# Kernel tuning notes

Hardware: AMD Instinct MI355X
Metric: run time of the kernel (lower is better)

The kernel has to match this reference:

```python
import jax, jax.numpy as jnp
import numpy as np

OHNM_RATIO = 30
DEFAULT_NEG_PERC = 0.1
EPS = 1e-10


def setup_inputs() -> dict:
    key = jax.random.key(0)
    k1, k2 = jax.random.split(key)
    shape = (1, 1, 256, 256, 256)  # (B, C, D, H, W) 3D segmentation volume
    preds = jax.random.normal(k1, shape, dtype=jnp.float32)  # raw logits
    targs = (jax.random.uniform(k2, shape, dtype=jnp.float32) < 1e-3).astype(jnp.int32)
    return {"preds": preds, "targs": targs}


def reference(preds, targs):
    t = targs.astype(preds.dtype)
    # elementwise BCE-with-logits: log(1 + e^x) - x * t  (numerically stable via logaddexp)
    losses = jnp.logaddexp(0.0, preds) - preds * t
    pf, tf, lf = preds.ravel(), t.ravel(), losses.ravel()

    # --- data-dependent hard-negative count (mirrors torch .item() host sync) ---
    n_pos = int(np.asarray(tf.sum()))
    n_neg = tf.size - n_pos
    n_hns = int(DEFAULT_NEG_PERC * n_neg) if n_pos == 0 else min(n_pos * OHNM_RATIO, n_neg)

    # mask out positives, take top-k hardest negatives over the flattened loss map
    masked = jnp.where(tf == 1.0, 0.0, lf)
    _, hns_idxs = jax.lax.top_k(masked, n_hns)
    # positive indices (data-dependent size, like torch.nonzero)
    pos_idxs = jnp.asarray(np.nonzero(np.asarray(tf) == 1.0)[0], dtype=hns_idxs.dtype)
    idxs = jnp.concatenate([hns_idxs, pos_idxs])  # [n_hns + n_pos]

    # gather selected samples, view as (B, C, -1) with B = C = 1
    ps = jax.nn.sigmoid(pf[idxs])[None, None, :]  # dice normalizes preds
    ts = tf[idxs][None, None, :]

    # Dice loss over dims 2+ (here the single flattened sample dim)
    inter = jnp.sum(ps * ts, axis=-1)              # [B, C]
    denom = jnp.sum(ps, axis=-1) + jnp.sum(ts, axis=-1)
    dice = jnp.mean(1.0 - (2.0 * inter + EPS) / (denom + EPS))

    return dice + jnp.mean(lf[idxs])
```

## Files before the change

kernel.cpp:

```cpp
#include <hip/hip_runtime.h>

#define EPSF 1e-10f

constexpr unsigned KEY15 = 0xBFC00000u;
constexpr int BUCK0 = 0xBFC;
constexpr int NB2   = 4096 - BUCK0;
constexpr int NBKT  = 4096;
constexpr int NREP  = 8;
constexpr int LHSZ  = NB2 + 64;

typedef float pf4 __attribute__((ext_vector_type(4)));
typedef int   pi4 __attribute__((ext_vector_type(4)));

constexpr int SC_OFF    = 0;
constexpr int BSTAT_OFF = 64;
constexpr int REP_OFF   = BSTAT_OFF + 4096 * 4;
constexpr int LOW_OFF   = REP_OFF + NREP * NB2;
constexpr int HF_OFF    = LOW_OFF + NBKT;
constexpr int ZERO_WORDS = LOW_OFF + NBKT;

__device__ __forceinline__ float sigmoidf_(float x) {
    return 1.0f / (1.0f + expf(-x));
}
__device__ __forceinline__ float softplusf_(float x) {
    return fmaxf(x, 0.0f) + log1pf(expf(-fabsf(x)));
}
__device__ __forceinline__ unsigned f2key(float x) {
    unsigned b = __float_as_uint(x);
    return b ^ ((unsigned)((int)b >> 31) | 0x80000000u);
}
__device__ __forceinline__ float key2f(unsigned k) {
    unsigned b = (k & 0x80000000u) ? (k & 0x7FFFFFFFu) : ~k;
    return __uint_as_float(b);
}

__global__ void zeroAll(unsigned* ws, int nwords) {
    int stride = gridDim.x * blockDim.x;
    for (int i = blockIdx.x * blockDim.x + threadIdx.x; i < nwords; i += stride)
        ws[i] = 0u;
}

__global__ __launch_bounds__(256) void k1(const float* __restrict__ preds,
                                          const int* __restrict__ targs, int N,
                                          float4* __restrict__ bstat,
                                          unsigned* __restrict__ rep) {
    __shared__ int lh[LHSZ];
    for (int i = threadIdx.x; i < LHSZ; i += 256) lh[i] = 0;
    __syncthreads();

    float pc = 0.f, psig = 0.f, plos = 0.f;
    const int tid = threadIdx.x;
    const int lane = tid & 63;
    const int w = tid >> 6;
    const int dummy = NB2 + lane;

    int nfull = N >> 13;
    for (int grp = blockIdx.x; grp < nfull; grp += gridDim.x) {
        size_t ebase = ((size_t)grp << 13) + ((size_t)w << 11) + ((size_t)lane << 2);
        const float* pp  = preds + ebase;
        const float* pp2 = pp + 1024;
        const int*   tp  = targs + ebase;
        const int*   tp2 = tp + 1024;
        pf4 P[8]; pi4 T[8];
        asm volatile(
            "global_load_dwordx4 %0, %16, off\n\t"
            "global_load_dwordx4 %1, %16, off offset:1024\n\t"
            "global_load_dwordx4 %2, %16, off offset:2048\n\t"
            "global_load_dwordx4 %3, %16, off offset:3072\n\t"
            "global_load_dwordx4 %4, %17, off\n\t"
            "global_load_dwordx4 %5, %17, off offset:1024\n\t"
            "global_load_dwordx4 %6, %17, off offset:2048\n\t"
            "global_load_dwordx4 %7, %17, off offset:3072\n\t"
            "global_load_dwordx4 %8, %18, off\n\t"
            "global_load_dwordx4 %9, %18, off offset:1024\n\t"
            "global_load_dwordx4 %10, %18, off offset:2048\n\t"
            "global_load_dwordx4 %11, %18, off offset:3072\n\t"
            "global_load_dwordx4 %12, %19, off\n\t"
            "global_load_dwordx4 %13, %19, off offset:1024\n\t"
            "global_load_dwordx4 %14, %19, off offset:2048\n\t"
            "global_load_dwordx4 %15, %19, off offset:3072\n\t"
            "s_waitcnt vmcnt(0)"
            : "=&v"(P[0]), "=&v"(P[1]), "=&v"(P[2]), "=&v"(P[3]),
              "=&v"(P[4]), "=&v"(P[5]), "=&v"(P[6]), "=&v"(P[7]),
              "=&v"(T[0]), "=&v"(T[1]), "=&v"(T[2]), "=&v"(T[3]),
              "=&v"(T[4]), "=&v"(T[5]), "=&v"(T[6]), "=&v"(T[7])
            : "v"(pp), "v"(pp2), "v"(tp), "v"(tp2)
            : "memory");
#pragma unroll
        for (int g = 0; g < 8; g++) {
            pf4 pv = P[g]; pi4 tv = T[g];
#pragma unroll
            for (int j = 0; j < 4; j++) {
                float x = pv[j];
                unsigned key = f2key(x);
                int bkt = (int)(key >> 20) - BUCK0;
                bool q = (key >= KEY15) & (tv[j] == 0);
                int addr = q ? bkt : dummy;
                atomicAdd(&lh[addr], 1);
            }
            if (tv[0] | tv[1] | tv[2] | tv[3]) {
#pragma unroll
                for (int j = 0; j < 4; j++)
                    if (tv[j]) {
                        float x = pv[j];
                        pc += 1.f; psig += sigmoidf_(x); plos += softplusf_(x) - x;
                    }
            }
        }
    }
    if (blockIdx.x == gridDim.x - 1) {
        for (int i = (nfull << 13) + tid; i < N; i += 256) {
            float x = preds[i];
            if (targs[i]) { pc += 1.f; psig += sigmoidf_(x); plos += softplusf_(x) - x; }
            else {
                unsigned key = f2key(x);
                if (key >= KEY15) atomicAdd(&lh[(key >> 20) - BUCK0], 1);
            }
        }
    }
    __syncthreads();
    float qc = 0.f;
    unsigned* my = rep + (unsigned)(blockIdx.x & (NREP - 1)) * NB2;
    for (int i = tid; i < NB2; i += 256) {
        int c = lh[i];
        if (c) { atomicAdd(&my[i], (unsigned)c); qc += (float)c; }
    }
#pragma unroll
    for (int o = 32; o > 0; o >>= 1) {
        pc   += __shfl_down(pc, o);
        psig += __shfl_down(psig, o);
        plos += __shfl_down(plos, o);
        qc   += __shfl_down(qc, o);
    }
    __shared__ float rp[4], rs[4], rl[4], rq[4];
    if ((tid & 63) == 0) { rp[w] = pc; rs[w] = psig; rl[w] = plos; rq[w] = qc; }
    __syncthreads();
    if (tid == 0)
        bstat[blockIdx.x] = make_float4(rp[0] + rp[1] + rp[2] + rp[3],
                                        rs[0] + rs[1] + rs[2] + rs[3],
                                        rl[0] + rl[1] + rl[2] + rl[3],
                                        rq[0] + rq[1] + rq[2] + rq[3]);
}

__global__ void flagK(const float4* __restrict__ bstat, int nblocks,
                      unsigned* __restrict__ sc, unsigned N) {
    float pc = 0.f, ps = 0.f, pl = 0.f, qt = 0.f;
    for (int i = threadIdx.x; i < nblocks; i += 256) {
        float4 v = bstat[i];
        pc += v.x; ps += v.y; pl += v.z; qt += v.w;
    }
#pragma unroll
    for (int o = 32; o > 0; o >>= 1) {
        pc += __shfl_down(pc, o);
        ps += __shfl_down(ps, o);
        pl += __shfl_down(pl, o);
        qt += __shfl_down(qt, o);
    }
    __shared__ float rp[4], rs[4], rl[4], rq[4];
    int w = threadIdx.x >> 6;
    if ((threadIdx.x & 63) == 0) { rp[w] = pc; rs[w] = ps; rl[w] = pl; rq[w] = qt; }
    __syncthreads();
    if (threadIdx.x == 0) {
        unsigned np = (unsigned)(rp[0] + rp[1] + rp[2] + rp[3] + 0.5f);
        float psT = rs[0] + rs[1] + rs[2] + rs[3];
        float plT = rl[0] + rl[1] + rl[2] + rl[3];
        unsigned qtT = (unsigned)(rq[0] + rq[1] + rq[2] + rq[3] + 0.5f);
        unsigned nn = N - np;
        unsigned k = (np == 0u) ? (unsigned)(0.1 * (double)nn)
                                : ((30u * np < nn) ? 30u * np : nn);
        float* scf = (float*)sc;
        sc[0] = np; scf[1] = psT; scf[2] = plT; sc[3] = k;
        sc[7] = (k > qtT) ? 1u : 0u;
    }
}

__global__ void redR(const unsigned* __restrict__ rep, unsigned* __restrict__ histF) {
    int i = blockIdx.x * 256 + threadIdx.x;
    if (i < NB2) {
        unsigned s0 = rep[0 * NB2 + i], s1 = rep[1 * NB2 + i];
        unsigned s2 = rep[2 * NB2 + i], s3 = rep[3 * NB2 + i];
        unsigned s4 = rep[4 * NB2 + i], s5 = rep[5 * NB2 + i];
        unsigned s6 = rep[6 * NB2 + i], s7 = rep[7 * NB2 + i];
        histF[i] = ((s0 + s1) + (s2 + s3)) + ((s4 + s5) + (s6 + s7));
    }
}

__global__ __launch_bounds__(256) void lowH(const float* __restrict__ preds,
                                            const int* __restrict__ targs, int N,
                                            const unsigned* __restrict__ sc,
                                            unsigned* __restrict__ low) {
    if (sc[7] == 0u) return;
    int gtid = blockIdx.x * 256 + threadIdx.x;
    int gstr = gridDim.x * 256;
    for (int i = gtid; i < N; i += gstr) {
        if (!targs[i]) {
            unsigned key = f2key(preds[i]);
            if (key < KEY15) atomicAdd(&low[key >> 20], 1u);
        }
    }
}

__global__ void finalize(const unsigned* __restrict__ histF,
                         const unsigned* __restrict__ low,
                         unsigned* __restrict__ sc, float* __restrict__ out) {
    __shared__ unsigned sa[256], sb[256];
    __shared__ int sb1;
    __shared__ unsigned sr1;
    __shared__ double rds[4], rdl[4];
    int t = threadIdx.x;
    int base = t * 16;
    unsigned c[16]; unsigned tot = 0;
#pragma unroll
    for (int j = 0; j < 16; j++) {
        int b = base + j;
        unsigned s = (b >= BUCK0) ? histF[b - BUCK0] : low[b];
        c[j] = s; tot += s;
    }
    sa[t] = tot;
    if (t == 0) { sb1 = NBKT; sr1 = 0u; }
    __syncthreads();
    unsigned k = sc[3];
    unsigned* src = sa; unsigned* dst = sb;
    for (int off = 1; off < 256; off <<= 1) {
        unsigned v = src[t] + ((t + off < 256) ? src[t + off] : 0u);
        dst[t] = v;
        __syncthreads();
        unsigned* tmp = src; src = dst; dst = tmp;
    }
    if (k > 0u) {
        unsigned above = src[t] - tot;
        if (above < k && above + tot >= k) {
            unsigned cum = above;
            for (int j = 15; j >= 0; j--) {
                unsigned cc = c[j];
                if (cum + cc >= k) { sb1 = base + j; sr1 = k - cum; break; }
                cum += cc;
            }
        }
    }
    __syncthreads();
    int b1 = sb1; unsigned r1 = sr1;
    double ssig = 0.0, ssp = 0.0;
#pragma unroll
    for (int j = 0; j < 16; j++) {
        int b = base + j; unsigned cc = c[j];
        if (cc == 0u) continue;
        bool full = (b > b1);
        bool part = (b == b1) && (r1 > 0u);
        if (!(full || part)) continue;
        float lo = key2f((unsigned)b << 20);
        float hi = (b == NBKT - 1) ? key2f(0xFF7FFFFFu)
                                   : key2f(((unsigned)(b + 1)) << 20);
        if (full) {
            float mid = 0.5f * (lo + hi);
            ssig += (double)cc * (double)sigmoidf_(mid);
            ssp  += (double)cc * (double)softplusf_(mid);
        } else {
            unsigned take = (r1 < cc) ? r1 : cc;
            double q = (double)take / (double)cc;
            float rp = (float)((double)hi - 0.5 * q * ((double)hi - (double)lo));
            ssig += (double)take * (double)sigmoidf_(rp);
            ssp  += (double)take * (double)softplusf_(rp);
        }
    }
#pragma unroll
    for (int o = 32; o > 0; o >>= 1) {
        ssig += __shfl_down(ssig, o);
        ssp  += __shfl_down(ssp, o);
    }
    int w = t >> 6;
    if ((t & 63) == 0) { rds[w] = ssig; rdl[w] = ssp; }
    __syncthreads();
    if (t == 0) {
        double sns = rds[0] + rds[1] + rds[2] + rds[3];
        double snl = rdl[0] + rdl[1] + rdl[2] + rdl[3];
        float* scf = (float*)sc;
        unsigned np = sc[0];
        float psig = scf[1], plos = scf[2];
        double denom = (double)psig + sns + (double)np;
        double dice = 1.0 - (2.0 * (double)psig + (double)EPSF) / (denom + (double)EPSF);
        unsigned totsel = np + k;
        double mean = totsel ? (((double)plos + snl) / (double)totsel) : 0.0;
        out[0] = (float)(dice + mean);
    }
}

extern "C" void kernel_launch(void* const* d_in, const int* in_sizes, int n_in,
                              void* d_out, int out_size, void* d_ws, size_t ws_size,
                              hipStream_t stream) {
    const float* preds = (const float*)d_in[0];
    const int*   targs = (const int*)d_in[1];
    float* out = (float*)d_out;
    int N = in_sizes[0];

    unsigned* ws    = (unsigned*)d_ws;
    unsigned* sc    = ws + SC_OFF;
    float4*   bstat = (float4*)(ws + BSTAT_OFF);
    unsigned* rep   = ws + REP_OFF;
    unsigned* low   = ws + LOW_OFF;
    unsigned* histF = ws + HF_OFF;

    int nfull = N >> 13;
    int grid = nfull + ((N & 8191) ? 1 : 0);
    if (grid < 1) grid = 1;
    if (grid > 4096) grid = 4096;

    zeroAll<<<64, 256, 0, stream>>>(ws, ZERO_WORDS);
    k1<<<grid, 256, 0, stream>>>(preds, targs, N, bstat, rep);
    flagK<<<1, 256, 0, stream>>>(bstat, grid, sc, (unsigned)N);
    lowH<<<512, 256, 0, stream>>>(preds, targs, N, sc, low);
    redR<<<(NB2 + 255) / 256, 256, 0, stream>>>(rep, histF);
    finalize<<<1, 256, 0, stream>>>(histF, low, sc, out);
}
```

Baseline: 161.3 us.

## Fuse histogram, flag, reduction and finalize into one last-block kernel

Merges the main histogram pass, the count/flag kernel, the replica reduction, the low-bucket fallback and the finalize step into a single kernel. The last block to finish, detected with an atomic ticket counter, performs all the tail work. This removes four kernel launches and the gaps between them. In exchange, the rare fallback scan over the low buckets now runs over all N elements in one block instead of 512 blocks. The block also carries a larger shared-memory footprint, which may reduce occupancy of the main pass.

```diff
diff --git a/kernel.cpp b/kernel.cpp
--- a/kernel.cpp
+++ b/kernel.cpp
@@ -16,8 +16,8 @@
 constexpr int BSTAT_OFF = 64;
 constexpr int REP_OFF   = BSTAT_OFF + 4096 * 4;
 constexpr int LOW_OFF   = REP_OFF + NREP * NB2;
-constexpr int HF_OFF    = LOW_OFF + NBKT;
-constexpr int ZERO_WORDS = LOW_OFF + NBKT;
+constexpr int ZERO_N    = NREP * NB2 + NBKT;
+constexpr int ZERO_TOT  = 64 + ZERO_N;
 
 __device__ __forceinline__ float sigmoidf_(float x) {
     return 1.0f / (1.0f + expf(-x));
@@ -34,17 +34,32 @@
     return __uint_as_float(b);
 }
 
-__global__ void zeroAll(unsigned* ws, int nwords) {
-    int stride = gridDim.x * blockDim.x;
-    for (int i = blockIdx.x * blockDim.x + threadIdx.x; i < nwords; i += stride)
-        ws[i] = 0u;
-}
-
-__global__ __launch_bounds__(256) void k1(const float* __restrict__ preds,
-                                          const int* __restrict__ targs, int N,
-                                          float4* __restrict__ bstat,
-                                          unsigned* __restrict__ rep) {
+__global__ void zeroAll(unsigned* ws) {
+    int stride = gridDim.x * 256;
+    for (int i = blockIdx.x * 256 + threadIdx.x; i < ZERO_TOT; i += stride)
+        ws[(i < 64) ? i : (REP_OFF - 64 + i)] = 0u;
+}
+
+__global__ __launch_bounds__(256) void fused(const float* __restrict__ preds,
+                                             const int* __restrict__ targs, int N,
+                                             unsigned* __restrict__ ws,
+                                             float* __restrict__ out) {
     __shared__ int lh[LHSZ];
+    __shared__ float rp[4], rs[4], rl[4], rq[4];
+    __shared__ unsigned histH[NB2];
+    __shared__ unsigned sa[256], sb[256];
+    __shared__ int sb1;
+    __shared__ unsigned sr1;
+    __shared__ double rds[4], rdl[4];
+    __shared__ int s_last;
+    __shared__ unsigned s_np, s_k, s_flag;
+    __shared__ float s_psig, s_plos;
+
+    unsigned* sc    = ws + SC_OFF;
+    float4*   bstat = (float4*)(ws + BSTAT_OFF);
+    unsigned* rep   = ws + REP_OFF;
+    unsigned* low   = ws + LOW_OFF;
+
     for (int i = threadIdx.x; i < LHSZ; i += 256) lh[i] = 0;
     __syncthreads();
 
@@ -132,156 +147,144 @@
         plos += __shfl_down(plos, o);
         qc   += __shfl_down(qc, o);
     }
-    __shared__ float rp[4], rs[4], rl[4], rq[4];
     if ((tid & 63) == 0) { rp[w] = pc; rs[w] = psig; rl[w] = plos; rq[w] = qc; }
     __syncthreads();
-    if (tid == 0)
+    if (tid == 0) {
         bstat[blockIdx.x] = make_float4(rp[0] + rp[1] + rp[2] + rp[3],
                                         rs[0] + rs[1] + rs[2] + rs[3],
                                         rl[0] + rl[1] + rl[2] + rl[3],
                                         rq[0] + rq[1] + rq[2] + rq[3]);
-}
-
-__global__ void flagK(const float4* __restrict__ bstat, int nblocks,
-                      unsigned* __restrict__ sc, unsigned N) {
-    float pc = 0.f, ps = 0.f, pl = 0.f, qt = 0.f;
-    for (int i = threadIdx.x; i < nblocks; i += 256) {
-        float4 v = bstat[i];
-        pc += v.x; ps += v.y; pl += v.z; qt += v.w;
-    }
-#pragma unroll
-    for (int o = 32; o > 0; o >>= 1) {
-        pc += __shfl_down(pc, o);
-        ps += __shfl_down(ps, o);
-        pl += __shfl_down(pl, o);
-        qt += __shfl_down(qt, o);
-    }
-    __shared__ float rp[4], rs[4], rl[4], rq[4];
-    int w = threadIdx.x >> 6;
-    if ((threadIdx.x & 63) == 0) { rp[w] = pc; rs[w] = ps; rl[w] = pl; rq[w] = qt; }
-    __syncthreads();
-    if (threadIdx.x == 0) {
-        unsigned np = (unsigned)(rp[0] + rp[1] + rp[2] + rp[3] + 0.5f);
-        float psT = rs[0] + rs[1] + rs[2] + rs[3];
-        float plT = rl[0] + rl[1] + rl[2] + rl[3];
-        unsigned qtT = (unsigned)(rq[0] + rq[1] + rq[2] + rq[3] + 0.5f);
-        unsigned nn = N - np;
-        unsigned k = (np == 0u) ? (unsigned)(0.1 * (double)nn)
-                                : ((30u * np < nn) ? 30u * np : nn);
-        float* scf = (float*)sc;
-        sc[0] = np; scf[1] = psT; scf[2] = plT; sc[3] = k;
-        sc[7] = (k > qtT) ? 1u : 0u;
-    }
-}
-
-__global__ void redR(const unsigned* __restrict__ rep, unsigned* __restrict__ histF) {
-    int i = blockIdx.x * 256 + threadIdx.x;
-    if (i < NB2) {
+        __threadfence();
+        unsigned t = atomicAdd(&sc[0], 1u);
+        s_last = (t == gridDim.x - 1) ? 1 : 0;
+    }
+    __syncthreads();
+    if (!s_last) return;
+    __threadfence();
+
+    {
+        float fpc = 0.f, fps = 0.f, fpl = 0.f, fqt = 0.f;
+        for (int i = tid; i < (int)gridDim.x; i += 256) {
+            float4 v = bstat[i];
+            fpc += v.x; fps += v.y; fpl += v.z; fqt += v.w;
+        }
+#pragma unroll
+        for (int o = 32; o > 0; o >>= 1) {
+            fpc += __shfl_down(fpc, o);
+            fps += __shfl_down(fps, o);
+            fpl += __shfl_down(fpl, o);
+            fqt += __shfl_down(fqt, o);
+        }
+        if ((tid & 63) == 0) { rp[w] = fpc; rs[w] = fps; rl[w] = fpl; rq[w] = fqt; }
+        __syncthreads();
+        if (tid == 0) {
+            unsigned np = (unsigned)(rp[0] + rp[1] + rp[2] + rp[3] + 0.5f);
+            float psT = rs[0] + rs[1] + rs[2] + rs[3];
+            float plT = rl[0] + rl[1] + rl[2] + rl[3];
+            unsigned qtT = (unsigned)(rq[0] + rq[1] + rq[2] + rq[3] + 0.5f);
+            unsigned nn = (unsigned)N - np;
+            unsigned k = (np == 0u) ? (unsigned)(0.1 * (double)nn)
+                                    : ((30u * np < nn) ? 30u * np : nn);
+            s_np = np; s_psig = psT; s_plos = plT; s_k = k;
+            s_flag = (k > qtT) ? 1u : 0u;
+        }
+        __syncthreads();
+    }
+
+    for (int i = tid; i < NB2; i += 256) {
         unsigned s0 = rep[0 * NB2 + i], s1 = rep[1 * NB2 + i];
         unsigned s2 = rep[2 * NB2 + i], s3 = rep[3 * NB2 + i];
         unsigned s4 = rep[4 * NB2 + i], s5 = rep[5 * NB2 + i];
         unsigned s6 = rep[6 * NB2 + i], s7 = rep[7 * NB2 + i];
-        histF[i] = ((s0 + s1) + (s2 + s3)) + ((s4 + s5) + (s6 + s7));
-    }
-}
-
-__global__ __launch_bounds__(256) void lowH(const float* __restrict__ preds,
-                                            const int* __restrict__ targs, int N,
-                                            const unsigned* __restrict__ sc,
-                                            unsigned* __restrict__ low) {
-    if (sc[7] == 0u) return;
-    int gtid = blockIdx.x * 256 + threadIdx.x;
-    int gstr = gridDim.x * 256;
-    for (int i = gtid; i < N; i += gstr) {
-        if (!targs[i]) {
-            unsigned key = f2key(preds[i]);
-            if (key < KEY15) atomicAdd(&low[key >> 20], 1u);
-        }
-    }
-}
-
-__global__ void finalize(const unsigned* __restrict__ histF,
-                         const unsigned* __restrict__ low,
-                         unsigned* __restrict__ sc, float* __restrict__ out) {
-    __shared__ unsigned sa[256], sb[256];
-    __shared__ int sb1;
-    __shared__ unsigned sr1;
-    __shared__ double rds[4], rdl[4];
-    int t = threadIdx.x;
-    int base = t * 16;
-    unsigned c[16]; unsigned tot = 0;
-#pragma unroll
-    for (int j = 0; j < 16; j++) {
-        int b = base + j;
-        unsigned s = (b >= BUCK0) ? histF[b - BUCK0] : low[b];
-        c[j] = s; tot += s;
-    }
-    sa[t] = tot;
-    if (t == 0) { sb1 = NBKT; sr1 = 0u; }
-    __syncthreads();
-    unsigned k = sc[3];
-    unsigned* src = sa; unsigned* dst = sb;
-    for (int off = 1; off < 256; off <<= 1) {
-        unsigned v = src[t] + ((t + off < 256) ? src[t + off] : 0u);
-        dst[t] = v;
-        __syncthreads();
-        unsigned* tmp = src; src = dst; dst = tmp;
-    }
-    if (k > 0u) {
-        unsigned above = src[t] - tot;
-        if (above < k && above + tot >= k) {
-            unsigned cum = above;
-            for (int j = 15; j >= 0; j--) {
-                unsigned cc = c[j];
-                if (cum + cc >= k) { sb1 = base + j; sr1 = k - cum; break; }
-                cum += cc;
-            }
-        }
-    }
-    __syncthreads();
-    int b1 = sb1; unsigned r1 = sr1;
-    double ssig = 0.0, ssp = 0.0;
-#pragma unroll
-    for (int j = 0; j < 16; j++) {
-        int b = base + j; unsigned cc = c[j];
-        if (cc == 0u) continue;
-        bool full = (b > b1);
-        bool part = (b == b1) && (r1 > 0u);
-        if (!(full || part)) continue;
-        float lo = key2f((unsigned)b << 20);
-        float hi = (b == NBKT - 1) ? key2f(0xFF7FFFFFu)
-                                   : key2f(((unsigned)(b + 1)) << 20);
-        if (full) {
-            float mid = 0.5f * (lo + hi);
-            ssig += (double)cc * (double)sigmoidf_(mid);
-            ssp  += (double)cc * (double)softplusf_(mid);
-        } else {
-            unsigned take = (r1 < cc) ? r1 : cc;
-            double q = (double)take / (double)cc;
-            float rp = (float)((double)hi - 0.5 * q * ((double)hi - (double)lo));
-            ssig += (double)take * (double)sigmoidf_(rp);
-            ssp  += (double)take * (double)softplusf_(rp);
-        }
-    }
-#pragma unroll
-    for (int o = 32; o > 0; o >>= 1) {
-        ssig += __shfl_down(ssig, o);
-        ssp  += __shfl_down(ssp, o);
-    }
-    int w = t >> 6;
-    if ((t & 63) == 0) { rds[w] = ssig; rdl[w] = ssp; }
-    __syncthreads();
-    if (t == 0) {
-        double sns = rds[0] + rds[1] + rds[2] + rds[3];
-        double snl = rdl[0] + rdl[1] + rdl[2] + rdl[3];
-        float* scf = (float*)sc;
-        unsigned np = sc[0];
-        float psig = scf[1], plos = scf[2];
-        double denom = (double)psig + sns + (double)np;
-        double dice = 1.0 - (2.0 * (double)psig + (double)EPSF) / (denom + (double)EPSF);
-        unsigned totsel = np + k;
-        double mean = totsel ? (((double)plos + snl) / (double)totsel) : 0.0;
-        out[0] = (float)(dice + mean);
+        histH[i] = ((s0 + s1) + (s2 + s3)) + ((s4 + s5) + (s6 + s7));
+    }
+
+    if (s_flag) {
+        for (int i = tid; i < N; i += 256) {
+            if (!targs[i]) {
+                unsigned key = f2key(preds[i]);
+                if (key < KEY15) atomicAdd(&low[key >> 20], 1u);
+            }
+        }
+    }
+    __syncthreads();
+
+    {
+        int t = tid;
+        int base = t * 16;
+        unsigned flag = s_flag;
+        unsigned c[16]; unsigned tot = 0;
+#pragma unroll
+        for (int j = 0; j < 16; j++) {
+            int b = base + j;
+            unsigned s = (b >= BUCK0) ? histH[b - BUCK0] : (flag ? low[b] : 0u);
+            c[j] = s; tot += s;
+        }
+        sa[t] = tot;
+        if (t == 0) { sb1 = NBKT; sr1 = 0u; }
+        __syncthreads();
+        unsigned k = s_k;
+        unsigned* src = sa; unsigned* dst = sb;
+        for (int off = 1; off < 256; off <<= 1) {
+            unsigned v = src[t] + ((t + off < 256) ? src[t + off] : 0u);
+            dst[t] = v;
+            __syncthreads();
+            unsigned* tmp = src; src = dst; dst = tmp;
+        }
+        if (k > 0u) {
+            unsigned above = src[t] - tot;
+            if (above < k && above + tot >= k) {
+                unsigned cum = above;
+                for (int j = 15; j >= 0; j--) {
+                    unsigned cc = c[j];
+                    if (cum + cc >= k) { sb1 = base + j; sr1 = k - cum; break; }
+                    cum += cc;
+                }
+            }
+        }
+        __syncthreads();
+        int b1 = sb1; unsigned r1 = sr1;
+        double ssig = 0.0, ssp = 0.0;
+#pragma unroll
+        for (int j = 0; j < 16; j++) {
+            int b = base + j; unsigned cc = c[j];
+            if (cc == 0u) continue;
+            bool full = (b > b1);
+            bool part = (b == b1) && (r1 > 0u);
+            if (!(full || part)) continue;
+            float lo = key2f((unsigned)b << 20);
+            float hi = (b == NBKT - 1) ? key2f(0xFF7FFFFFu)
+                                       : key2f(((unsigned)(b + 1)) << 20);
+            if (full) {
+                float mid = 0.5f * (lo + hi);
+                ssig += (double)cc * (double)sigmoidf_(mid);
+                ssp  += (double)cc * (double)softplusf_(mid);
+            } else {
+                unsigned take = (r1 < cc) ? r1 : cc;
+                double q = (double)take / (double)cc;
+                float rpv = (float)((double)hi - 0.5 * q * ((double)hi - (double)lo));
+                ssig += (double)take * (double)sigmoidf_(rpv);
+                ssp  += (double)take * (double)softplusf_(rpv);
+            }
+        }
+#pragma unroll
+        for (int o = 32; o > 0; o >>= 1) {
+            ssig += __shfl_down(ssig, o);
+            ssp  += __shfl_down(ssp, o);
+        }
+        if ((t & 63) == 0) { rds[w] = ssig; rdl[w] = ssp; }
+        __syncthreads();
+        if (t == 0) {
+            double sns = rds[0] + rds[1] + rds[2] + rds[3];
+            double snl = rdl[0] + rdl[1] + rdl[2] + rdl[3];
+            unsigned np = s_np;
+            float psig2 = s_psig, plos2 = s_plos;
+            double denom = (double)psig2 + sns + (double)np;
+            double dice = 1.0 - (2.0 * (double)psig2 + (double)EPSF) / (denom + (double)EPSF);
+            unsigned totsel = np + k;
+            double mean = totsel ? (((double)plos2 + snl) / (double)totsel) : 0.0;
+            out[0] = (float)(dice + mean);
+        }
     }
 }
 
@@ -292,23 +295,13 @@
     const int*   targs = (const int*)d_in[1];
     float* out = (float*)d_out;
     int N = in_sizes[0];
-
-    unsigned* ws    = (unsigned*)d_ws;
-    unsigned* sc    = ws + SC_OFF;
-    float4*   bstat = (float4*)(ws + BSTAT_OFF);
-    unsigned* rep   = ws + REP_OFF;
-    unsigned* low   = ws + LOW_OFF;
-    unsigned* histF = ws + HF_OFF;
+    unsigned* ws = (unsigned*)d_ws;
 
     int nfull = N >> 13;
     int grid = nfull + ((N & 8191) ? 1 : 0);
     if (grid < 1) grid = 1;
     if (grid > 4096) grid = 4096;
 
-    zeroAll<<<64, 256, 0, stream>>>(ws, ZERO_WORDS);
-    k1<<<grid, 256, 0, stream>>>(preds, targs, N, bstat, rep);
-    flagK<<<1, 256, 0, stream>>>(bstat, grid, sc, (unsigned)N);
-    lowH<<<512, 256, 0, stream>>>(preds, targs, N, sc, low);
-    redR<<<(NB2 + 255) / 256, 256, 0, stream>>>(rep, histF);
-    finalize<<<1, 256, 0, stream>>>(histF, low, sc, out);
-}
+    zeroAll<<<64, 256, 0, stream>>>(ws);
+    fused<<<grid, 256, 0, stream>>>(preds, targs, N, ws, out);
+}
```

Measured after the change: 251.0 us. 1.56x slower.
